# Performance work log

Measured on AMD Instinct MI355X. Metric: run time of the kernel, lower is better.

Reference implementation:

```python
import jax, jax.numpy as jnp
import numpy as np

B, F, N = 16, 128, 20000  # batch, feature (edge==node==message size), num nodes
M = F  # message_size = edge_feature_size


def setup_inputs() -> dict:
    key = jax.random.key(0)
    ks = jax.random.split(key, 9)
    s = 1.0 / np.sqrt(F)
    return {
        "h_w": jax.random.normal(ks[0], (B, F, N), jnp.float32),
        "h_v": jax.random.normal(ks[1], (B, F), jnp.float32),
        "e_wv": jax.random.normal(ks[2], (B, F, N), jnp.float32),
        "W_e2m": jax.random.normal(ks[3], (M, F), jnp.float32) * s,
        "b_e2m": jax.random.normal(ks[4], (M,), jnp.float32) * s,
        "W_n2m": jax.random.normal(ks[5], (M, F), jnp.float32) * s,
        "b_n2m": jax.random.normal(ks[6], (M,), jnp.float32) * s,
        "W_resize": jax.random.normal(ks[7], (M, 3 * M), jnp.float32) * (1.0 / np.sqrt(3 * M)),
        "b_resize": jax.random.normal(ks[8], (M,), jnp.float32) * (1.0 / np.sqrt(3 * M)),
    }


def reference(h_w, h_v, e_wv, W_e2m, b_e2m, W_n2m, b_n2m, W_resize, b_resize):
    # Per-node loop vectorized over the node axis n.
    # tmp_msg = cat([e2m(e_wv[:,:,n]), n2m(h_w[:,:,n]), n2m(h_v)], dim=1)
    # message[:,:,n] = resize_m(tmp_msg)
    # Split W_resize into its three column blocks to avoid materializing the
    # [B, 3M, N] concat: resize(cat(a,b,c)) = Wa@a + Wb@b + Wc@c + b.
    Wa = W_resize[:, :M]          # acts on e2m output
    Wb = W_resize[:, M:2 * M]     # acts on n2m(h_w)
    Wc = W_resize[:, 2 * M:]      # acts on n2m(h_v)

    em = jnp.einsum('bfn,mf->bmn', e_wv, W_e2m) + b_e2m[:, None]   # [B,M,N]
    nw = jnp.einsum('bfn,mf->bmn', h_w, W_n2m) + b_n2m[:, None]    # [B,M,N]
    nv = h_v @ W_n2m.T + b_n2m                                      # [B,M]

    msg = (jnp.einsum('bmn,km->bkn', em, Wa)
           + jnp.einsum('bmn,km->bkn', nw, Wb)
           + ((nv @ Wc.T) + b_resize)[:, :, None])                  # [B,M,N]
    return msg
```

## Files before the change

kernel.cpp:

```cpp
#include <hip/hip_runtime.h>
#include <hip/hip_bf16.h>

typedef __attribute__((ext_vector_type(8))) short bf16x8;
typedef __attribute__((ext_vector_type(4))) float f32x4;

#define F_DIM 128
#define N_DIM 20000
#define M_DIM 128
#define NW 32
#define TILES_PER_B 625
#define NT 20
#define GRID 500
#define F32_TILE 32768
#define F32_MAT 16384
#define BF16_OFF 65536
#define BF16_MAT 8192

#define AS1 __attribute__((address_space(1)))
#define AS3 __attribute__((address_space(3)))

static __device__ inline unsigned short f2bf(float x) {
    union { float f; unsigned u; } v; v.f = x;
    unsigned r = v.u + 0x7fffu + ((v.u >> 16) & 1u);
    return (unsigned short)(r >> 16);
}

static __device__ inline unsigned cvt_pk_bf16(float lo, float hi) {
    unsigned r;
    asm("v_cvt_pk_bf16_f32 %0, %1, %2" : "=v"(r) : "v"(lo), "v"(hi));
    return r;
}

__global__ __launch_bounds__(256) void precompute_mats(
    const float* __restrict__ W_rs,
    const float* __restrict__ W_e2m,
    const float* __restrict__ W_n2m,
    unsigned short* __restrict__ wsA,
    unsigned short* __restrict__ wsB)
{
    int idx = blockIdx.x * 256 + threadIdx.x;
    int k = idx >> 7;
    int f = idx & 127;
    float a = 0.f, b = 0.f;
    for (int m = 0; m < 128; ++m) {
        a += W_rs[k * 384 + m]       * W_e2m[m * 128 + f];
        b += W_rs[k * 384 + 128 + m] * W_n2m[m * 128 + f];
    }
    int mt = k >> 4, row = k & 15;
    int c = f >> 5, kk = f & 31;
    int lane = ((kk >> 3) << 4) | row;
    int j = kk & 7;
    int off = ((mt * 4 + c) * 64 + lane) * 8 + j;
    wsA[off] = f2bf(a);
    wsB[off] = f2bf(b);
}

__global__ __launch_bounds__(128) void precompute_bias(
    const float* __restrict__ W_rs,
    const float* __restrict__ h_v,
    const float* __restrict__ b_e2m,
    const float* __restrict__ b_n2m,
    const float* __restrict__ b_rs,
    const float* __restrict__ W_n2m,
    float* __restrict__ bias)
{
    __shared__ float nv_s[128];
    int b = blockIdx.x;
    int t = threadIdx.x;
    {
        float nv = b_n2m[t];
        for (int f = 0; f < 128; ++f)
            nv += h_v[b * 128 + f] * W_n2m[t * 128 + f];
        nv_s[t] = nv;
    }
    __syncthreads();
    {
        float acc = b_rs[t];
        for (int m = 0; m < 128; ++m) {
            acc += W_rs[t * 384 + m]       * b_e2m[m];
            acc += W_rs[t * 384 + 128 + m] * b_n2m[m];
            acc += W_rs[t * 384 + 256 + m] * nv_s[m];
        }
        bias[b * 128 + t] = acc;
    }
}

__global__ __launch_bounds__(256, 2) void msg_main(
    const float* __restrict__ e_wv,
    const float* __restrict__ h_w,
    const unsigned short* __restrict__ wsA,
    const unsigned short* __restrict__ wsB,
    const float* __restrict__ bias,
    float* __restrict__ out)
{
    __shared__ __align__(16) unsigned char smem[81920];

    int tid = threadIdx.x;
    int w   = tid >> 6;
    int l   = tid & 63;
    unsigned base = (unsigned)blockIdx.x * NT;

    const bf16x8* Af = (const bf16x8*)wsA;
    const bf16x8* Bf = (const bf16x8*)wsB;
    bf16x8 A0[4], A1[4], B0[4], B1[4];
#pragma unroll
    for (int c = 0; c < 4; ++c) {
        A0[c] = Af[((2 * w + 0) * 4 + c) * 64 + l];
        A1[c] = Af[((2 * w + 1) * 4 + c) * 64 + l];
        B0[c] = Bf[((2 * w + 0) * 4 + c) * 64 + l];
        B1[c] = Bf[((2 * w + 1) * 4 + c) * 64 + l];
    }

    int fl = l >> 3, p = l & 7;
    auto issue_dma = [&](unsigned tau, unsigned bufsel) {
        unsigned bb = tau / TILES_PER_B;
        unsigned n0 = (tau - bb * TILES_PER_B) * NW;
        const float* eb = e_wv + (size_t)bb * (F_DIM * (size_t)N_DIM) + n0;
        const float* wp = h_w  + (size_t)bb * (F_DIM * (size_t)N_DIM) + n0;
        unsigned char* buf = smem + bufsel * F32_TILE;
#pragma unroll
        for (int i = 0; i < 4; ++i) {
            int fb = i * 32 + w * 8;
            int f  = fb + fl;
            int g  = (f ^ (f >> 3)) & 7;
            int col = (p ^ g) << 2;
            __builtin_amdgcn_global_load_lds(
                (const AS1 unsigned*)(eb + (size_t)f * N_DIM + col),
                (AS3 unsigned*)(buf + fb * 128), 16, 0, 0);
            __builtin_amdgcn_global_load_lds(
                (const AS1 unsigned*)(wp + (size_t)f * N_DIM + col),
                (AS3 unsigned*)(buf + F32_MAT + fb * 128), 16, 0, 0);
        }
    };

    auto issue_dma_dummy = [&](unsigned bufsel) {
        unsigned char* buf = smem + bufsel * F32_TILE;
#pragma unroll
        for (int i = 0; i < 4; ++i) {
            int fb = i * 32 + w * 8;
            __builtin_amdgcn_global_load_lds(
                (const AS1 unsigned*)e_wv,
                (AS3 unsigned*)(buf + fb * 128), 16, 0, 0);
            __builtin_amdgcn_global_load_lds(
                (const AS1 unsigned*)h_w,
                (AS3 unsigned*)(buf + F32_MAT + fb * 128), 16, 0, 0);
        }
    };

    auto transform = [&](unsigned bufsel) {
        const unsigned char* fsrc = smem + bufsel * F32_TILE + (tid >> 7) * F32_MAT;
        unsigned char* bdst = smem + BF16_OFF + (tid >> 7) * BF16_MAT;
        int u = tid & 127;
        int fp = u >> 1, half = u & 1;
        int f0 = 2 * fp, f1 = 2 * fp + 1;
        int g0 = (f0 ^ (f0 >> 3)) & 7, g1 = (f1 ^ (f1 >> 3)) & 7;
#pragma unroll
        for (int j = 0; j < 4; ++j) {
            int q = half * 4 + j;
            f32x4 a = *(const f32x4*)(fsrc + f0 * 128 + ((q ^ g0) << 4));
            f32x4 c = *(const f32x4*)(fsrc + f1 * 128 + ((q ^ g1) << 4));
#pragma unroll
            for (int e = 0; e < 4; ++e) {
                int n = q * 4 + e;
                unsigned pk = cvt_pk_bf16(a[e], c[e]);
                unsigned off = (unsigned)(n * 256) +
                               (((unsigned)(fp * 4)) ^ ((unsigned)((n & 7) << 4)));
                *(unsigned*)(bdst + off) = pk;
            }
        }
    };

    issue_dma(base + 0, 0);
    issue_dma(base + 1, 1);
    asm volatile("s_waitcnt vmcnt(8)" ::: "memory");
    __builtin_amdgcn_s_barrier();
    transform(0);
    asm volatile("s_waitcnt lgkmcnt(0)" ::: "memory");
    __builtin_amdgcn_s_barrier();

    int ln = l & 15, g = l >> 4;
    unsigned rbase = (unsigned)(ln * 256);
    unsigned rx = (unsigned)((ln & 7) << 4);
    const unsigned char* ldse = smem + BF16_OFF;
    const unsigned char* ldsw = smem + BF16_OFF + BF16_MAT;

#pragma unroll 1
    for (int t = 0; t < NT; ++t) {
        unsigned tau = base + t;
        unsigned bb = tau / TILES_PER_B;
        unsigned n0 = (tau - bb * TILES_PER_B) * NW;

        const float* bp = bias + bb * 128;
        f32x4 bv0 = *(const f32x4*)(bp + (2 * w + 0) * 16 + g * 4);
        f32x4 bv1 = *(const f32x4*)(bp + (2 * w + 1) * 16 + g * 4);

        if (t < NT - 2) issue_dma(base + t + 2, (unsigned)(t & 1));
        else            issue_dma_dummy((unsigned)(t & 1));

        f32x4 acc[2][2];
#pragma unroll
        for (int mtL = 0; mtL < 2; ++mtL)
#pragma unroll
            for (int ns = 0; ns < 2; ++ns) acc[mtL][ns] = (f32x4)(0.f);
#pragma unroll
        for (int c = 0; c < 4; ++c) {
            unsigned fbyte = (unsigned)((c * 32 + g * 8) * 2) ^ rx;
#pragma unroll
            for (int ns = 0; ns < 2; ++ns) {
                bf16x8 xe = *(const bf16x8*)(ldse + ns * 4096 + rbase + fbyte);
                bf16x8 xw = *(const bf16x8*)(ldsw + ns * 4096 + rbase + fbyte);
                acc[0][ns] = __builtin_amdgcn_mfma_f32_16x16x32_bf16(A0[c], xe, acc[0][ns], 0, 0, 0);
                acc[0][ns] = __builtin_amdgcn_mfma_f32_16x16x32_bf16(B0[c], xw, acc[0][ns], 0, 0, 0);
                acc[1][ns] = __builtin_amdgcn_mfma_f32_16x16x32_bf16(A1[c], xe, acc[1][ns], 0, 0, 0);
                acc[1][ns] = __builtin_amdgcn_mfma_f32_16x16x32_bf16(B1[c], xw, acc[1][ns], 0, 0, 0);
            }
        }

        if (t == 0) { asm volatile("s_waitcnt vmcnt(8)"  ::: "memory"); }
        else        { asm volatile("s_waitcnt vmcnt(24)" ::: "memory"); }
        asm volatile("s_waitcnt lgkmcnt(0)" ::: "memory");
        __builtin_amdgcn_s_barrier();

        if (t < NT - 1) transform((unsigned)((t + 1) & 1));
        asm volatile("s_waitcnt lgkmcnt(0)" ::: "memory");
        __builtin_amdgcn_s_barrier();

        float* O = out + (size_t)bb * (M_DIM * (size_t)N_DIM) + n0 + ln;
#pragma unroll
        for (int mtL = 0; mtL < 2; ++mtL) {
            f32x4 bv = mtL ? bv1 : bv0;
            int mt = 2 * w + mtL;
#pragma unroll
            for (int ns = 0; ns < 2; ++ns)
#pragma unroll
                for (int r = 0; r < 4; ++r)
                    O[(size_t)(mt * 16 + g * 4 + r) * N_DIM + ns * 16] =
                        acc[mtL][ns][r] + bv[r];
        }
    }

    asm volatile("s_waitcnt vmcnt(0)" ::: "memory");
}

extern "C" void kernel_launch(void* const* d_in, const int* in_sizes, int n_in,
                              void* d_out, int out_size, void* d_ws, size_t ws_size,
                              hipStream_t stream) {
    const float* h_w   = (const float*)d_in[0];
    const float* h_v   = (const float*)d_in[1];
    const float* e_wv  = (const float*)d_in[2];
    const float* W_e2m = (const float*)d_in[3];
    const float* b_e2m = (const float*)d_in[4];
    const float* W_n2m = (const float*)d_in[5];
    const float* b_n2m = (const float*)d_in[6];
    const float* W_rs  = (const float*)d_in[7];
    const float* b_rs  = (const float*)d_in[8];
    float* out = (float*)d_out;

    unsigned short* wsA = (unsigned short*)d_ws;
    unsigned short* wsB = wsA + 128 * 128;
    float* bias = (float*)((char*)d_ws + 65536);

    precompute_mats<<<64, 256, 0, stream>>>(W_rs, W_e2m, W_n2m, wsA, wsB);
    precompute_bias<<<16, 128, 0, stream>>>(W_rs, h_v, b_e2m, b_n2m, b_rs, W_n2m, bias);
    msg_main<<<GRID, 256, 0, stream>>>(e_wv, h_w, wsA, wsB, bias, out);
}
```

Measured before the change: 134.5 us.

## Halve node tile width, double grid and occupancy, and swizzle block order

Shrinks each node tile from 32 to 16 columns, which halves the LDS footprint so four blocks fit per CU, and doubles the grid to 1000 blocks. The DMA, transform swizzles and vmcnt wait counts are re-derived for the narrower tile. Blocks are also remapped with an XCD-style interleave, so neighbouring tiles land on different dies. The aim is more latency hiding through occupancy, at the cost of 64-byte row segments that are less efficient for global loads and stores, and less MFMA work per barrier.

```diff
diff --git a/kernel.cpp b/kernel.cpp
--- a/kernel.cpp
+++ b/kernel.cpp
@@ -7,14 +7,14 @@
 #define F_DIM 128
 #define N_DIM 20000
 #define M_DIM 128
-#define NW 32
-#define TILES_PER_B 625
+#define NW 16
+#define TILES_PER_B 1250
 #define NT 20
-#define GRID 500
-#define F32_TILE 32768
-#define F32_MAT 16384
-#define BF16_OFF 65536
-#define BF16_MAT 8192
+#define GRID 1000
+#define F32_MAT 8192
+#define F32_TILE 16384
+#define BF16_OFF 32768
+#define BF16_MAT 4096
 
 #define AS1 __attribute__((address_space(1)))
 #define AS3 __attribute__((address_space(3)))
@@ -85,7 +85,7 @@
     }
 }
 
-__global__ __launch_bounds__(256, 2) void msg_main(
+__global__ __launch_bounds__(256, 4) void msg_main(
     const float* __restrict__ e_wv,
     const float* __restrict__ h_w,
     const unsigned short* __restrict__ wsA,
@@ -93,12 +93,14 @@
     const float* __restrict__ bias,
     float* __restrict__ out)
 {
-    __shared__ __align__(16) unsigned char smem[81920];
+    __shared__ __align__(16) unsigned char smem[40960];
 
     int tid = threadIdx.x;
     int w   = tid >> 6;
     int l   = tid & 63;
-    unsigned base = (unsigned)blockIdx.x * NT;
+    int blk0 = blockIdx.x;
+    int blk  = (blk0 & 7) * (GRID / 8) + (blk0 >> 3);
+    unsigned base = (unsigned)blk * NT;
 
     const bf16x8* Af = (const bf16x8*)wsA;
     const bf16x8* Bf = (const bf16x8*)wsB;
@@ -111,7 +113,7 @@
         B1[c] = Bf[((2 * w + 1) * 4 + c) * 64 + l];
     }
 
-    int fl = l >> 3, p = l & 7;
+    int fl = l >> 2, p = l & 3;
     auto issue_dma = [&](unsigned tau, unsigned bufsel) {
         unsigned bb = tau / TILES_PER_B;
         unsigned n0 = (tau - bb * TILES_PER_B) * NW;
@@ -119,31 +121,31 @@
         const float* wp = h_w  + (size_t)bb * (F_DIM * (size_t)N_DIM) + n0;
         unsigned char* buf = smem + bufsel * F32_TILE;
 #pragma unroll
-        for (int i = 0; i < 4; ++i) {
-            int fb = i * 32 + w * 8;
+        for (int i = 0; i < 2; ++i) {
+            int fb = i * 64 + w * 16;
             int f  = fb + fl;
-            int g  = (f ^ (f >> 3)) & 7;
+            int g  = (f ^ (f >> 2)) & 3;
             int col = (p ^ g) << 2;
             __builtin_amdgcn_global_load_lds(
                 (const AS1 unsigned*)(eb + (size_t)f * N_DIM + col),
-                (AS3 unsigned*)(buf + fb * 128), 16, 0, 0);
+                (AS3 unsigned*)(buf + fb * 64), 16, 0, 0);
             __builtin_amdgcn_global_load_lds(
                 (const AS1 unsigned*)(wp + (size_t)f * N_DIM + col),
-                (AS3 unsigned*)(buf + F32_MAT + fb * 128), 16, 0, 0);
+                (AS3 unsigned*)(buf + F32_MAT + fb * 64), 16, 0, 0);
         }
     };
 
     auto issue_dma_dummy = [&](unsigned bufsel) {
         unsigned char* buf = smem + bufsel * F32_TILE;
 #pragma unroll
-        for (int i = 0; i < 4; ++i) {
-            int fb = i * 32 + w * 8;
+        for (int i = 0; i < 2; ++i) {
+            int fb = i * 64 + w * 16;
             __builtin_amdgcn_global_load_lds(
                 (const AS1 unsigned*)e_wv,
-                (AS3 unsigned*)(buf + fb * 128), 16, 0, 0);
+                (AS3 unsigned*)(buf + fb * 64), 16, 0, 0);
             __builtin_amdgcn_global_load_lds(
                 (const AS1 unsigned*)h_w,
-                (AS3 unsigned*)(buf + F32_MAT + fb * 128), 16, 0, 0);
+                (AS3 unsigned*)(buf + F32_MAT + fb * 64), 16, 0, 0);
         }
     };
 
@@ -153,12 +155,12 @@
         int u = tid & 127;
         int fp = u >> 1, half = u & 1;
         int f0 = 2 * fp, f1 = 2 * fp + 1;
-        int g0 = (f0 ^ (f0 >> 3)) & 7, g1 = (f1 ^ (f1 >> 3)) & 7;
-#pragma unroll
-        for (int j = 0; j < 4; ++j) {
-            int q = half * 4 + j;
-            f32x4 a = *(const f32x4*)(fsrc + f0 * 128 + ((q ^ g0) << 4));
-            f32x4 c = *(const f32x4*)(fsrc + f1 * 128 + ((q ^ g1) << 4));
+        int g0 = (f0 ^ (f0 >> 2)) & 3, g1 = (f1 ^ (f1 >> 2)) & 3;
+#pragma unroll
+        for (int j = 0; j < 2; ++j) {
+            int q = half * 2 + j;
+            f32x4 a = *(const f32x4*)(fsrc + f0 * 64 + ((q ^ g0) << 4));
+            f32x4 c = *(const f32x4*)(fsrc + f1 * 64 + ((q ^ g1) << 4));
 #pragma unroll
             for (int e = 0; e < 4; ++e) {
                 int n = q * 4 + e;
@@ -172,7 +174,7 @@
 
     issue_dma(base + 0, 0);
     issue_dma(base + 1, 1);
-    asm volatile("s_waitcnt vmcnt(8)" ::: "memory");
+    asm volatile("s_waitcnt vmcnt(4)" ::: "memory");
     __builtin_amdgcn_s_barrier();
     transform(0);
     asm volatile("s_waitcnt lgkmcnt(0)" ::: "memory");
@@ -197,27 +199,22 @@
         if (t < NT - 2) issue_dma(base + t + 2, (unsigned)(t & 1));
         else            issue_dma_dummy((unsigned)(t & 1));
 
-        f32x4 acc[2][2];
-#pragma unroll
-        for (int mtL = 0; mtL < 2; ++mtL)
-#pragma unroll
-            for (int ns = 0; ns < 2; ++ns) acc[mtL][ns] = (f32x4)(0.f);
+        f32x4 acc[2];
+        acc[0] = (f32x4)(0.f);
+        acc[1] = (f32x4)(0.f);
 #pragma unroll
         for (int c = 0; c < 4; ++c) {
             unsigned fbyte = (unsigned)((c * 32 + g * 8) * 2) ^ rx;
-#pragma unroll
-            for (int ns = 0; ns < 2; ++ns) {
-                bf16x8 xe = *(const bf16x8*)(ldse + ns * 4096 + rbase + fbyte);
-                bf16x8 xw = *(const bf16x8*)(ldsw + ns * 4096 + rbase + fbyte);
-                acc[0][ns] = __builtin_amdgcn_mfma_f32_16x16x32_bf16(A0[c], xe, acc[0][ns], 0, 0, 0);
-                acc[0][ns] = __builtin_amdgcn_mfma_f32_16x16x32_bf16(B0[c], xw, acc[0][ns], 0, 0, 0);
-                acc[1][ns] = __builtin_amdgcn_mfma_f32_16x16x32_bf16(A1[c], xe, acc[1][ns], 0, 0, 0);
-                acc[1][ns] = __builtin_amdgcn_mfma_f32_16x16x32_bf16(B1[c], xw, acc[1][ns], 0, 0, 0);
-            }
-        }
-
-        if (t == 0) { asm volatile("s_waitcnt vmcnt(8)"  ::: "memory"); }
-        else        { asm volatile("s_waitcnt vmcnt(24)" ::: "memory"); }
+            bf16x8 xe = *(const bf16x8*)(ldse + rbase + fbyte);
+            bf16x8 xw = *(const bf16x8*)(ldsw + rbase + fbyte);
+            acc[0] = __builtin_amdgcn_mfma_f32_16x16x32_bf16(A0[c], xe, acc[0], 0, 0, 0);
+            acc[0] = __builtin_amdgcn_mfma_f32_16x16x32_bf16(B0[c], xw, acc[0], 0, 0, 0);
+            acc[1] = __builtin_amdgcn_mfma_f32_16x16x32_bf16(A1[c], xe, acc[1], 0, 0, 0);
+            acc[1] = __builtin_amdgcn_mfma_f32_16x16x32_bf16(B1[c], xw, acc[1], 0, 0, 0);
+        }
+
+        if (t == 0) { asm volatile("s_waitcnt vmcnt(6)"  ::: "memory"); }
+        else        { asm volatile("s_waitcnt vmcnt(14)" ::: "memory"); }
         asm volatile("s_waitcnt lgkmcnt(0)" ::: "memory");
         __builtin_amdgcn_s_barrier();
 
@@ -231,11 +228,8 @@
             f32x4 bv = mtL ? bv1 : bv0;
             int mt = 2 * w + mtL;
 #pragma unroll
-            for (int ns = 0; ns < 2; ++ns)
-#pragma unroll
-                for (int r = 0; r < 4; ++r)
-                    O[(size_t)(mt * 16 + g * 4 + r) * N_DIM + ns * 16] =
-                        acc[mtL][ns][r] + bv[r];
+            for (int r = 0; r < 4; ++r)
+                O[(size_t)(mt * 16 + g * 4 + r) * N_DIM] = acc[mtL][r] + bv[r];
         }
     }
 
```

Result: slower. 163.2 us (+21.3%).
